# Optimization experiments

Measured on AMD Instinct MI355X. Metric: run time of the kernel, lower is better.

The kernel has to match this reference:

```python
import jax, jax.numpy as jnp
import numpy as np

EPS = 1e-5  # torch BatchNorm2d default eps

# BinaryActivation with STE: grad zeroed where |x| >= 1 (the extra 1.3 clip in
# xnor_binarize.backward is a subset and thus redundant).
@jax.custom_vjp
def sign_act(x):
    return jnp.sign(x)

def _sa_fwd(x):
    return jnp.sign(x), x

def _sa_bwd(x, g):
    mask = ((x > -1.0) & (x < 1.0)).astype(g.dtype)
    return (g * mask,)

sign_act.defvjp(_sa_fwd, _sa_bwd)

# Weight binarization (scale=False path): w.data.clamp_(-1,1) then sign();
# backward is straight-through identity (|bi_weight|=1 < 1.3 so clip never fires).
@jax.custom_vjp
def bin_weight(w):
    return jnp.sign(jnp.clip(w, -1.0, 1.0))

def _bw_fwd(w):
    return jnp.sign(jnp.clip(w, -1.0, 1.0)), None

def _bw_bwd(_, g):
    return (g,)

bin_weight.defvjp(_bw_fwd, _bw_bwd)


def _branch(x, gamma, beta, w, bias):
    # BatchNorm2d (training-mode batch stats, biased var), affine
    mu = jnp.mean(x, axis=(0, 2, 3), keepdims=True)
    var = jnp.var(x, axis=(0, 2, 3), keepdims=True)
    h = (x - mu) * jax.lax.rsqrt(var + EPS)
    h = h * gamma[None, :, None, None] + beta[None, :, None, None]
    # XNOR conv: binarized activations and weights, stride 2, pad 1
    a = sign_act(h)
    bw = bin_weight(w)
    y = jax.lax.conv_general_dilated(
        a, bw, window_strides=(2, 2), padding=[(1, 1), (1, 1)],
        dimension_numbers=('NCHW', 'OIHW', 'NCHW'))
    y = y + bias[None, :, None, None]
    # shortcut: AvgPool2d(kernel_size=2) (stride defaults to 2)
    B, C, H, W = x.shape
    sc = x.reshape(B, C, H // 2, 2, W // 2, 2).mean(axis=(3, 5))
    return jax.nn.relu(y) + sc


def setup_inputs() -> dict:
    key = jax.random.key(0)
    ks = jax.random.split(key, 9)
    B, C, H, W = 32, 192, 64, 64
    K = 3
    x = jax.random.normal(ks[0], (B, C, H, W), dtype=jnp.float32)
    g1 = 1.0 + 0.1 * jax.random.normal(ks[1], (C,), dtype=jnp.float32)
    b1 = 0.1 * jax.random.normal(ks[2], (C,), dtype=jnp.float32)
    w1 = 0.05 * jax.random.normal(ks[3], (C, C, K, K), dtype=jnp.float32)
    bias1 = jnp.zeros((C,), dtype=jnp.float32)
    g2 = 1.0 + 0.1 * jax.random.normal(ks[4], (C,), dtype=jnp.float32)
    b2 = 0.1 * jax.random.normal(ks[5], (C,), dtype=jnp.float32)
    w2 = 0.05 * jax.random.normal(ks[6], (C, C, K, K), dtype=jnp.float32)
    bias2 = jnp.zeros((C,), dtype=jnp.float32)
    return {"x": x, "g1": g1, "b1": b1, "w1": w1, "bias1": bias1,
            "g2": g2, "b2": b2, "w2": w2, "bias2": bias2}


def reference(x, g1, b1, w1, bias1, g2, b2, w2, bias2):
    x1 = _branch(x, g1, b1, w1, bias1)
    x2 = _branch(x, g2, b2, w2, bias2)
    return jnp.concatenate([x1, x2], axis=1)  # [B, 2C, H/2, W/2]
```

## Files before the change

kernel.cpp:

```cpp
#include <hip/hip_runtime.h>

typedef unsigned int u32;

#define BN 32
#define CC 192
#define HH 64
#define WW 64
#define HWSZ (HH*WW)
#define OHH 32
#define OWW 32
#define NVALID_SCALE 131072.0f
#define PLH 65
#define PLW2 66
#define PLSZ (PLH*PLW2)
#define NPLANE (12*BN)
#define NSTATS (CC*BN)
#define NPW (2*CC)
#define WSTR 12

__global__ __launch_bounds__(256) void k_front(const float* __restrict__ x,
        float* __restrict__ partial,
        const float* __restrict__ w1, const float* __restrict__ w2,
        u32* __restrict__ wp, u32* __restrict__ wsum,
        u32* __restrict__ act) {
    __shared__ float red[8];
    __shared__ float wl[CC * 9];
    __shared__ u32 ww[54];
    int blk = blockIdx.x;
    int tid = threadIdx.x;
    if (blk < NSTATS) {
        int c = blk >> 5, n = blk & 31;
        const float4* p = (const float4*)(x + ((size_t)(n * CC + c) << 12));
        float s = 0.f, s2 = 0.f;
#pragma unroll
        for (int k = 0; k < 4; ++k) {
            float4 f = p[tid + 256 * k];
            s  += f.x + f.y + f.z + f.w;
            s2 += f.x * f.x + f.y * f.y + f.z * f.z + f.w * f.w;
        }
#pragma unroll
        for (int off = 32; off > 0; off >>= 1) {
            s  += __shfl_down(s, off, 64);
            s2 += __shfl_down(s2, off, 64);
        }
        int wv = tid >> 6, ln = tid & 63;
        if (ln == 0) { red[wv * 2] = s; red[wv * 2 + 1] = s2; }
        __syncthreads();
        if (tid == 0) {
            partial[blk * 2]     = red[0] + red[2] + red[4] + red[6];
            partial[blk * 2 + 1] = red[1] + red[3] + red[5] + red[7];
        }
    } else if (blk < NSTATS + NPW) {
        int b  = blk - NSTATS;
        int br = b / CC, oc = b - br * CC;
        const float* W = (br ? w2 : w1) + (size_t)oc * CC * 9;
        for (int i = tid; i < CC * 9; i += 256) wl[i] = W[i];
        __syncthreads();
        if (tid < 72) {
            int w6 = tid / 12, pos = tid % 12;
            u32 word = 0;
            if (pos < 9) {
#pragma unroll
                for (int bb = 0; bb < 32; ++bb) {
                    if (wl[(w6 * 32 + bb) * 9 + pos] > 0.f) word |= (1u << bb);
                }
                ww[w6 * 9 + pos] = word;
            }
            wp[((size_t)(br * 6 + w6) * CC + oc) * WSTR + pos] = word;
        }
        __syncthreads();
        if (tid == 0) {
            int Wt[9];
#pragma unroll
            for (int t = 0; t < 9; ++t) {
                int s = 0;
#pragma unroll
                for (int w6 = 0; w6 < 6; ++w6) s += __popc(ww[w6 * 9 + t]);
                Wt[t] = s;
            }
            wsum[b * 4 + 0] = (u32)(Wt[0] + Wt[1] + Wt[2]);
            wsum[b * 4 + 1] = (u32)(Wt[0] + Wt[3] + Wt[6]);
            wsum[b * 4 + 2] = (u32)Wt[0];
            wsum[b * 4 + 3] = 0;
        }
    } else {
        int plane = blk - NSTATS - NPW;
        u32* pl = act + (size_t)plane * PLSZ;
        if (tid < PLW2) pl[tid] = 0;
        else if (tid < PLW2 + 64) pl[(tid - PLW2 + 1) * PLW2 + 1] = 0;
    }
}

__global__ __launch_bounds__(64) void k_coef(const float* __restrict__ partial,
        const float* __restrict__ g1, const float* __restrict__ b1,
        const float* __restrict__ g2, const float* __restrict__ b2,
        float* __restrict__ coef) {
    int c = blockIdx.x;
    int t = threadIdx.x;
    int half = t >> 5, i = t & 31;
    float v = partial[(c * 32 + i) * 2 + half];
#pragma unroll
    for (int off = 16; off > 0; off >>= 1) v += __shfl_down(v, off, 32);
    float S2 = __shfl(v, 32, 64);
    if (t == 0) {
        float S = v;
        const float inv = 1.0f / NVALID_SCALE;
        float mu  = S * inv;
        float var = S2 * inv - mu * mu;
        float r   = 1.0f / sqrtf(var + 1e-5f);
        float s1 = g1[c] * r, t1 = b1[c] - mu * s1;
        float s2 = g2[c] * r, t2 = b2[c] - mu * s2;
        ((float4*)coef)[c] = make_float4(s1, t1, s2, t2);
    }
}

__global__ __launch_bounds__(256) void k_pack_act(const float* __restrict__ x,
        const float* __restrict__ coef, u32* __restrict__ act,
        float* __restrict__ scb) {
    int bx = blockIdx.x;
    int g  = blockIdx.y;
    int n = bx >> 2, q = bx & 3;
    int tid = threadIdx.x;
    int ow = tid & 31, oh = (q << 3) + (tid >> 5);
    const float4* c4 = (const float4*)coef;
    const float* xb = x + (size_t)n * CC * HWSZ + (size_t)(2 * oh) * WW + 2 * ow;
    float* scp = scb + ((size_t)(n * CC + g * 32) * OHH + oh) * OWW + ow;
    u32 pk[8] = {0, 0, 0, 0, 0, 0, 0, 0};
#pragma unroll 4
    for (int bb = 0; bb < 32; ++bb) {
        int ch = g * 32 + bb;
        const float* p = xb + (size_t)ch * HWSZ;
        float2 r0 = *(const float2*)p;
        float2 r1 = *(const float2*)(p + WW);
        scp[(size_t)bb * (OHH * OWW)] = (r0.x + r0.y + r1.x + r1.y) * 0.25f;
        float4 cf = c4[ch];
        u32 bit = 1u << bb;
        if (r0.x * cf.x + cf.y > 0.f) pk[0] |= bit;
        if (r0.y * cf.x + cf.y > 0.f) pk[1] |= bit;
        if (r1.x * cf.x + cf.y > 0.f) pk[2] |= bit;
        if (r1.y * cf.x + cf.y > 0.f) pk[3] |= bit;
        if (r0.x * cf.z + cf.w > 0.f) pk[4] |= bit;
        if (r0.y * cf.z + cf.w > 0.f) pk[5] |= bit;
        if (r1.x * cf.z + cf.w > 0.f) pk[6] |= bit;
        if (r1.y * cf.z + cf.w > 0.f) pk[7] |= bit;
    }
    size_t o00 = (size_t)(2 * oh + 1) * PLW2 + (2 * ow + 2);
    u32* a1 = act + ((size_t)(0 * 6 + g) * BN + n) * PLSZ + o00;
    u32* a2 = act + ((size_t)(1 * 6 + g) * BN + n) * PLSZ + o00;
    *(uint2*)a1            = make_uint2(pk[0], pk[1]);
    *(uint2*)(a1 + PLW2)   = make_uint2(pk[2], pk[3]);
    *(uint2*)a2            = make_uint2(pk[4], pk[5]);
    *(uint2*)(a2 + PLW2)   = make_uint2(pk[6], pk[7]);
}

__global__ __launch_bounds__(256) void k_conv(
        const u32* __restrict__ act, const u32* __restrict__ wp,
        const uint4* __restrict__ wsum4, const float* __restrict__ scb,
        const float* __restrict__ bias1, const float* __restrict__ bias2,
        float* __restrict__ out) {
    int b    = blockIdx.x;
    int tile = b >> 2;
    int n    = tile >> 4, ohp = tile & 15;
    int wid  = __builtin_amdgcn_readfirstlane((int)(threadIdx.x >> 6));
    int ocbase = ((b & 3) * 4 + wid) * 12;
    int lane = threadIdx.x & 63;
    int ow = lane & 31, lh = lane >> 5;
    int oh = 2 * ohp + lh;
    int lbase = (2 * oh) * PLW2 + 2 * ow + 1;
    int topE  = (oh == 0), leftE = (ow == 0);
    int nv192 = CC * ((topE ? 2 : 3) * (leftE ? 2 : 3));
#pragma unroll 1
    for (int br = 0; br < 2; ++br) {
        int p[12];
#pragma unroll
        for (int j = 0; j < 12; ++j) p[j] = 0;
        const u32* ap  = act + ((size_t)(br * 6) * BN + n) * PLSZ + lbase;
        const u32* wqb = wp + ((size_t)(br * 6) * CC + ocbase) * WSTR;
#pragma unroll 2
        for (int w6 = 0; w6 < 6; ++w6) {
            const u32* app = ap + (size_t)w6 * (BN * PLSZ);
            u32 a[9];
#pragma unroll
            for (int t = 0; t < 9; ++t) a[t] = app[(t / 3) * PLW2 + (t % 3)];
            const u32* wr = wqb + (size_t)w6 * (CC * WSTR);
#pragma unroll
            for (int j = 0; j < 12; ++j) {
#pragma unroll
                for (int t = 0; t < 9; ++t) {
                    p[j] += __popc(a[t] ^ wr[j * WSTR + t]);
                }
            }
        }
        const uint4*  ws4 = wsum4 + (br * CC + ocbase);
        const float*  bsp = (br ? bias2 : bias1) + ocbase;
#pragma unroll
        for (int j = 0; j < 12; ++j) {
            uint4 wsv = ws4[j];
            int corr = (topE ? (int)wsv.x : 0) + (leftE ? (int)wsv.y : 0)
                     - ((topE & leftE) ? (int)wsv.z : 0);
            int dot = nv192 - 2 * p[j] + 2 * corr;
            int oc = ocbase + j;
            float y = (float)dot + bsp[j];
            float sc = scb[((size_t)(n * CC + oc) * OHH + oh) * OWW + ow];
            __builtin_nontemporal_store(fmaxf(y, 0.f) + sc,
                &out[((size_t)(n * 384 + br * CC + oc) * OHH + oh) * OWW + ow]);
        }
    }
}

extern "C" void kernel_launch(void* const* d_in, const int* in_sizes, int n_in,
                              void* d_out, int out_size, void* d_ws, size_t ws_size,
                              hipStream_t stream) {
    const float* x     = (const float*)d_in[0];
    const float* g1    = (const float*)d_in[1];
    const float* b1    = (const float*)d_in[2];
    const float* w1    = (const float*)d_in[3];
    const float* bias1 = (const float*)d_in[4];
    const float* g2    = (const float*)d_in[5];
    const float* b2    = (const float*)d_in[6];
    const float* w2    = (const float*)d_in[7];
    const float* bias2 = (const float*)d_in[8];
    float* out = (float*)d_out;
    char* ws = (char*)d_ws;
    float* partial = (float*)(ws);
    float* coef    = (float*)(ws + 49152);
    u32*   wp      = (u32*)  (ws + 52224);
    u32*   wsum    = (u32*)  (ws + 162816);
    float* scb     = (float*)(ws + 168960);
    u32*   act     = (u32*)  (ws + 25334784);

    hipLaunchKernelGGL(k_front,   dim3(NSTATS + NPW + NPLANE), dim3(256), 0, stream,
                       x, partial, w1, w2, wp, wsum, act);
    hipLaunchKernelGGL(k_coef,    dim3(CC),          dim3(64),  0, stream,
                       partial, g1, b1, g2, b2, coef);
    hipLaunchKernelGGL(k_pack_act, dim3(128, 6),     dim3(256), 0, stream,
                       x, coef, act, scb);
    hipLaunchKernelGGL(k_conv,    dim3(BN * 16 * 4), dim3(256), 0, stream,
                       act, wp, (const uint4*)wsum, scb, bias1, bias2, out);
}
```

Baseline: 242.8 us.

## Fuse BN coefficient computation into activation packing and split channel loop across lanes

Removes the separate k_coef launch. Each pack block now reduces the partial sums for its 32 channels into shared memory. The packing kernel splits the 32-channel loop into two 16-channel halves per wave and merges the bit masks with a cross-lane xor shuffle, doubling the grid to expose more parallelism. The conv kernel hoists its shortcut loads out of the branch loop so they are read once instead of twice. The cost is redundant coefficient reduction across blocks and extra registers in conv.

```diff
diff --git a/kernel.cpp b/kernel.cpp
--- a/kernel.cpp
+++ b/kernel.cpp
@@ -91,49 +91,51 @@
     }
 }
 
-__global__ __launch_bounds__(64) void k_coef(const float* __restrict__ partial,
+__global__ __launch_bounds__(256) void k_pack_act(const float* __restrict__ x,
+        const float* __restrict__ partial,
         const float* __restrict__ g1, const float* __restrict__ b1,
         const float* __restrict__ g2, const float* __restrict__ b2,
-        float* __restrict__ coef) {
-    int c = blockIdx.x;
-    int t = threadIdx.x;
-    int half = t >> 5, i = t & 31;
-    float v = partial[(c * 32 + i) * 2 + half];
-#pragma unroll
-    for (int off = 16; off > 0; off >>= 1) v += __shfl_down(v, off, 32);
-    float S2 = __shfl(v, 32, 64);
-    if (t == 0) {
-        float S = v;
-        const float inv = 1.0f / NVALID_SCALE;
-        float mu  = S * inv;
-        float var = S2 * inv - mu * mu;
-        float r   = 1.0f / sqrtf(var + 1e-5f);
-        float s1 = g1[c] * r, t1 = b1[c] - mu * s1;
-        float s2 = g2[c] * r, t2 = b2[c] - mu * s2;
-        ((float4*)coef)[c] = make_float4(s1, t1, s2, t2);
-    }
-}
-
-__global__ __launch_bounds__(256) void k_pack_act(const float* __restrict__ x,
-        const float* __restrict__ coef, u32* __restrict__ act,
-        float* __restrict__ scb) {
+        u32* __restrict__ act, float* __restrict__ scb) {
     int bx = blockIdx.x;
     int g  = blockIdx.y;
-    int n = bx >> 2, q = bx & 3;
+    int n = bx >> 3, q = bx & 7;
     int tid = threadIdx.x;
-    int ow = tid & 31, oh = (q << 3) + (tid >> 5);
-    const float4* c4 = (const float4*)coef;
+    __shared__ float4 cf_s[32];
+    if (tid < 128) {
+        int ch = tid >> 2, k = tid & 3;
+        int c = g * 32 + ch;
+        int half = k >> 1, i0 = (k & 1) << 4;
+        float s = 0.f;
+#pragma unroll
+        for (int i = 0; i < 16; ++i) s += partial[(c * 32 + i0 + i) * 2 + half];
+        s += __shfl_xor(s, 1, 64);
+        float S2 = __shfl_down(s, 2, 64);
+        if (k == 0) {
+            float S = s;
+            const float inv = 1.0f / NVALID_SCALE;
+            float mu  = S * inv;
+            float var = S2 * inv - mu * mu;
+            float r   = 1.0f / sqrtf(var + 1e-5f);
+            float s1 = g1[c] * r, t1 = b1[c] - mu * s1;
+            float s2 = g2[c] * r, t2 = b2[c] - mu * s2;
+            cf_s[ch] = make_float4(s1, t1, s2, t2);
+        }
+    }
+    __syncthreads();
+    int wave = tid >> 6, lane = tid & 63;
+    int ow = lane & 31, chh = lane >> 5;
+    int oh = q * 4 + wave;
     const float* xb = x + (size_t)n * CC * HWSZ + (size_t)(2 * oh) * WW + 2 * ow;
-    float* scp = scb + ((size_t)(n * CC + g * 32) * OHH + oh) * OWW + ow;
+    float* scp = scb + ((size_t)(n * CC + g * 32 + chh * 16) * OHH + oh) * OWW + ow;
     u32 pk[8] = {0, 0, 0, 0, 0, 0, 0, 0};
 #pragma unroll 4
-    for (int bb = 0; bb < 32; ++bb) {
-        int ch = g * 32 + bb;
-        const float* p = xb + (size_t)ch * HWSZ;
+    for (int i = 0; i < 16; ++i) {
+        int bb = chh * 16 + i;
+        const float* p = xb + (size_t)(g * 32 + bb) * HWSZ;
         float2 r0 = *(const float2*)p;
         float2 r1 = *(const float2*)(p + WW);
-        scp[(size_t)bb * (OHH * OWW)] = (r0.x + r0.y + r1.x + r1.y) * 0.25f;
-        float4 cf = c4[ch];
+        scp[(size_t)i * (OHH * OWW)] = (r0.x + r0.y + r1.x + r1.y) * 0.25f;
+        float4 cf = cf_s[bb];
         u32 bit = 1u << bb;
         if (r0.x * cf.x + cf.y > 0.f) pk[0] |= bit;
         if (r0.y * cf.x + cf.y > 0.f) pk[1] |= bit;
@@ -144,13 +146,17 @@
         if (r1.x * cf.z + cf.w > 0.f) pk[6] |= bit;
         if (r1.y * cf.z + cf.w > 0.f) pk[7] |= bit;
     }
-    size_t o00 = (size_t)(2 * oh + 1) * PLW2 + (2 * ow + 2);
-    u32* a1 = act + ((size_t)(0 * 6 + g) * BN + n) * PLSZ + o00;
-    u32* a2 = act + ((size_t)(1 * 6 + g) * BN + n) * PLSZ + o00;
-    *(uint2*)a1            = make_uint2(pk[0], pk[1]);
-    *(uint2*)(a1 + PLW2)   = make_uint2(pk[2], pk[3]);
-    *(uint2*)a2            = make_uint2(pk[4], pk[5]);
-    *(uint2*)(a2 + PLW2)   = make_uint2(pk[6], pk[7]);
+#pragma unroll
+    for (int r = 0; r < 8; ++r) pk[r] |= __shfl_xor(pk[r], 32, 64);
+    if (chh == 0) {
+        size_t o00 = (size_t)(2 * oh + 1) * PLW2 + (2 * ow + 2);
+        u32* a1 = act + ((size_t)(0 * 6 + g) * BN + n) * PLSZ + o00;
+        u32* a2 = act + ((size_t)(1 * 6 + g) * BN + n) * PLSZ + o00;
+        *(uint2*)a1            = make_uint2(pk[0], pk[1]);
+        *(uint2*)(a1 + PLW2)   = make_uint2(pk[2], pk[3]);
+        *(uint2*)a2            = make_uint2(pk[4], pk[5]);
+        *(uint2*)(a2 + PLW2)   = make_uint2(pk[6], pk[7]);
+    }
 }
 
 __global__ __launch_bounds__(256) void k_conv(
@@ -169,6 +175,11 @@
     int lbase = (2 * oh) * PLW2 + 2 * ow + 1;
     int topE  = (oh == 0), leftE = (ow == 0);
     int nv192 = CC * ((topE ? 2 : 3) * (leftE ? 2 : 3));
+    float sc[12];
+#pragma unroll
+    for (int j = 0; j < 12; ++j) {
+        sc[j] = scb[((size_t)(n * CC + ocbase + j) * OHH + oh) * OWW + ow];
+    }
 #pragma unroll 1
     for (int br = 0; br < 2; ++br) {
         int p[12];
@@ -201,8 +212,7 @@
             int dot = nv192 - 2 * p[j] + 2 * corr;
             int oc = ocbase + j;
             float y = (float)dot + bsp[j];
-            float sc = scb[((size_t)(n * CC + oc) * OHH + oh) * OWW + ow];
-            __builtin_nontemporal_store(fmaxf(y, 0.f) + sc,
+            __builtin_nontemporal_store(fmaxf(y, 0.f) + sc[j],
                 &out[((size_t)(n * 384 + br * CC + oc) * OHH + oh) * OWW + ow]);
         }
     }
@@ -223,18 +233,15 @@
     float* out = (float*)d_out;
     char* ws = (char*)d_ws;
     float* partial = (float*)(ws);
-    float* coef    = (float*)(ws + 49152);
-    u32*   wp      = (u32*)  (ws + 52224);
-    u32*   wsum    = (u32*)  (ws + 162816);
-    float* scb     = (float*)(ws + 168960);
-    u32*   act     = (u32*)  (ws + 25334784);
-
-    hipLaunchKernelGGL(k_front,   dim3(NSTATS + NPW + NPLANE), dim3(256), 0, stream,
+    u32*   wp      = (u32*)  (ws + 49152);
+    u32*   wsum    = (u32*)  (ws + 159744);
+    float* scb     = (float*)(ws + 165888);
+    u32*   act     = (u32*)  (ws + 25331712);
+
+    hipLaunchKernelGGL(k_front,    dim3(NSTATS + NPW + NPLANE), dim3(256), 0, stream,
                        x, partial, w1, w2, wp, wsum, act);
-    hipLaunchKernelGGL(k_coef,    dim3(CC),          dim3(64),  0, stream,
-                       partial, g1, b1, g2, b2, coef);
-    hipLaunchKernelGGL(k_pack_act, dim3(128, 6),     dim3(256), 0, stream,
-                       x, coef, act, scb);
-    hipLaunchKernelGGL(k_conv,    dim3(BN * 16 * 4), dim3(256), 0, stream,
+    hipLaunchKernelGGL(k_pack_act, dim3(BN * 8, 6),  dim3(256), 0, stream,
+                       x, partial, g1, b1, g2, b2, act, scb);
+    hipLaunchKernelGGL(k_conv,     dim3(BN * 16 * 4), dim3(256), 0, stream,
                        act, wp, (const uint4*)wsum, scb, bias1, bias2, out);
 }
```

After: 241.5 us. No clear change (-0.5%).
